# Optimization experiments

Hardware: AMD Instinct MI355X
Metric: run time of the kernel (lower is better)

The kernel has to match this reference:

```python
import jax, jax.numpy as jnp
import numpy as np

N = 100000   # nodes
E = 600000   # edges
B = 512      # graphs in batch
H = 128      # hidden dim
ED = 8       # edge feature dim
TWO48 = float(2 ** 48 - 1)


def _w(k, shape, fan_in):
    return jax.random.normal(k, shape, jnp.float32) * (1.0 / np.sqrt(fan_in))


def setup_inputs() -> dict:
    key = jax.random.key(0)
    ks = jax.random.split(key, 32)
    inp = {}
    inp["s_node_ids"] = jax.random.randint(ks[0], (N,), 0, 2 ** 31 - 1, dtype=jnp.int32)
    inp["s_edge_index"] = jax.random.randint(ks[1], (2, E), 0, N, dtype=jnp.int32)
    inp["s_edge_attr"] = jax.random.normal(ks[2], (E, ED), jnp.float32)
    inp["s_batch"] = jnp.sort(jax.random.randint(ks[3], (N,), 0, B, dtype=jnp.int32))
    inp["depth"] = jax.random.uniform(ks[4], (B,), jnp.float32)
    # id_mlp: Linear(1,H) -> ReLU -> Linear(H,H)
    inp["id_w1"] = _w(ks[5], (1, H), 1); inp["id_b1"] = jnp.zeros((H,), jnp.float32)
    inp["id_w2"] = _w(ks[6], (H, H), H); inp["id_b2"] = jnp.zeros((H,), jnp.float32)
    # edge_mlp: Linear(ED,H) -> ReLU -> Linear(H,H)
    inp["ed_w1"] = _w(ks[7], (ED, H), ED); inp["ed_b1"] = jnp.zeros((H,), jnp.float32)
    inp["ed_w2"] = _w(ks[8], (H, H), H); inp["ed_b2"] = jnp.zeros((H,), jnp.float32)
    # GINEConv nn MLPs: Linear(H,H) -> ReLU -> Linear(H,H)
    inp["c1_w1"] = _w(ks[9], (H, H), H); inp["c1_b1"] = jnp.zeros((H,), jnp.float32)
    inp["c1_w2"] = _w(ks[10], (H, H), H); inp["c1_b2"] = jnp.zeros((H,), jnp.float32)
    inp["c2_w1"] = _w(ks[11], (H, H), H); inp["c2_b1"] = jnp.zeros((H,), jnp.float32)
    inp["c2_w2"] = _w(ks[12], (H, H), H); inp["c2_b2"] = jnp.zeros((H,), jnp.float32)
    inp["rg_w1"] = _w(ks[13], (H + 1, H), H + 1); inp["rg_b1"] = jnp.zeros((H,), jnp.float32)
    inp["rg_w2"] = _w(ks[14], (H, 1), H); inp["rg_b2"] = jnp.zeros((1,), jnp.float32)
    return inp


def _mlp2(x, w1, b1, w2, b2):
    return jax.nn.relu(x @ w1 + b1) @ w2 + b2


def _gine(x, src, dst, e, w1, b1, w2, b2):
    # message = ReLU(x_j + e), sum-aggregated at dst; out = nn((1+eps)*x + aggr), eps=0
    msg = jax.nn.relu(x[src] + e)                       # [E, H]
    aggr = jax.ops.segment_sum(msg, dst, num_segments=N)  # [N, H]
    return _mlp2(x + aggr, w1, b1, w2, b2)


def _global_mean(x, batch):
    sums = jax.ops.segment_sum(x, batch, num_segments=B)                          # [B, H]
    cnts = jax.ops.segment_sum(jnp.ones((x.shape[0], 1), x.dtype), batch, num_segments=B)
    return sums / jnp.maximum(cnts, 1.0)


def reference(s_node_ids, s_edge_index, s_edge_attr, s_batch, depth,
              id_w1, id_b1, id_w2, id_b2,
              ed_w1, ed_b1, ed_w2, ed_b2,
              c1_w1, c1_b1, c1_w2, c1_b2,
              c2_w1, c2_b1, c2_w2, c2_b2,
              rg_w1, rg_b1, rg_w2, rg_b2):
    src, dst = s_edge_index[0], s_edge_index[1]
    x0 = jnp.clip(s_node_ids.astype(jnp.float32) / TWO48, 0.0, 1.0)[:, None]  # [N,1]
    x = _mlp2(x0, id_w1, id_b1, id_w2, id_b2)                                 # [N,H]
    e = _mlp2(s_edge_attr, ed_w1, ed_b1, ed_w2, ed_b2)                        # [E,H]
    x = jax.nn.relu(_gine(x, src, dst, e, c1_w1, c1_b1, c1_w2, c1_b2))
    x = jax.nn.relu(_gine(x, src, dst, e, c2_w1, c2_b1, c2_w2, c2_b2))
    rep = jnp.concatenate([_global_mean(x, s_batch), depth[:, None]], axis=1)  # [B,H+1]
    return _mlp2(rep, rg_w1, rg_b1, rg_w2, rg_b2)[:, 0]                        # [B]
```

## Files before the change

### kernel.cpp

```cpp
#include <hip/hip_runtime.h>
#include <hip/hip_bf16.h>

#define N_NODES 100000
#define N_EDGES 600000
#define NB      512
#define H       128
#define ED      8
#define SCAN_CHUNK 1024
#define N_CHUNKS   98

typedef __attribute__((ext_vector_type(8))) short short8;
typedef __attribute__((ext_vector_type(4))) float f32x4;
typedef __attribute__((ext_vector_type(4))) unsigned int u32x4;
typedef unsigned short u16;
typedef unsigned int   u32;

static __device__ __forceinline__ u16 f2bf(float f) {
    u32 u = __float_as_uint(f);
    u32 r = u + 0x7fffu + ((u >> 16) & 1u);
    return (u16)(r >> 16);
}
static __device__ __forceinline__ float bf2f(u32 h) {
    return __uint_as_float(h << 16);
}
static __device__ __forceinline__ u32 bfpack(float lo, float hi) {
    u32 r;
    asm("v_cvt_pk_bf16_f32 %0, %1, %2" : "=v"(r) : "v"(lo), "v"(hi));
    return r;
}

__global__ __launch_bounds__(256) void pack_hist_kernel(
    const float* __restrict__ W0, const float* __restrict__ W1,
    const float* __restrict__ W2, const float* __restrict__ W3,
    const float* __restrict__ W4, const float* __restrict__ W5,
    const float* __restrict__ W6,
    short8* __restrict__ O0, short8* __restrict__ O1,
    short8* __restrict__ O2, short8* __restrict__ O3,
    short8* __restrict__ O4, short8* __restrict__ O5,
    short8* __restrict__ O6,
    const int* __restrict__ edge_index, int* __restrict__ counts)
{
    if (blockIdx.x >= 50) {
        int e = (blockIdx.x - 50) * 256 + threadIdx.x;
        if (e < N_EDGES) atomicAdd(&counts[edge_index[N_EDGES + e]], 1);
        return;
    }
    int gid = blockIdx.x * 256 + threadIdx.x;
    const float* W; short8* O; int Krows, kkmax, slot;
    if (gid < 512) { W = W0; O = O0; Krows = ED; kkmax = 1; slot = gid; }
    else {
        int m = (gid - 512) / 2048;
        slot = (gid - 512) % 2048;
        Krows = H; kkmax = 4;
        switch (m) {
            case 0: W = W1; O = O1; break;
            case 1: W = W2; O = O2; break;
            case 2: W = W3; O = O3; break;
            case 3: W = W4; O = O4; break;
            case 4: W = W5; O = O5; break;
            default: W = W6; O = O6; break;
        }
    }
    int lane = slot & 63;
    int t = slot >> 6;
    int nt = t & 1; t >>= 1;
    int kk = t % kkmax;
    int w  = t / kkmax;
    int quad = lane >> 4, n15 = lane & 15;
    int n = w * 32 + nt * 16 + n15;
    short8 v;
    #pragma unroll
    for (int j = 0; j < 8; j++) {
        int k = kk * 32 + quad * 8 + j;
        v[j] = (k < Krows) ? (short)f2bf(W[k * H + n]) : (short)0;
    }
    O[slot] = v;
}

__global__ __launch_bounds__(256) void scan_node_kernel(
    const int* __restrict__ counts, int* __restrict__ chunk_scan,
    int* __restrict__ bsum_raw,
    const int* __restrict__ ids,
    const float* __restrict__ w1, const float* __restrict__ b1,
    const short8* __restrict__ pW2, const float* __restrict__ b2,
    u16* __restrict__ x_out)
{
    __shared__ u16 sH[64 * 136];
    __shared__ float s_x0[64];
    __shared__ int sS[256];
    int tid = threadIdx.x;

    if (blockIdx.x < N_CHUNKS) {
        int base = blockIdx.x * SCAN_CHUNK + tid * 4;
        int4 v = *(const int4*)&counts[base];
        int q0 = v.x, q1 = q0 + v.y, q2 = q1 + v.z, q3 = q2 + v.w;
        sS[tid] = q3;
        __syncthreads();
        #pragma unroll
        for (int off = 1; off < 256; off <<= 1) {
            int t = (tid >= off) ? sS[tid - off] : 0;
            __syncthreads();
            sS[tid] += t;
            __syncthreads();
        }
        int excl = sS[tid] - q3;
        int4 o;
        o.x = excl; o.y = excl + q0; o.z = excl + q1; o.w = excl + q2;
        *(int4*)&chunk_scan[base] = o;
        if (tid == 255) bsum_raw[blockIdx.x] = sS[255];
        return;
    }

    int bid = blockIdx.x - N_CHUNKS;
    int w = tid >> 6, lane = tid & 63, quad = lane >> 4, n15 = lane & 15;
    short8 fW2[4][2];
    #pragma unroll
    for (int kk = 0; kk < 4; kk++) {
        fW2[kk][0] = pW2[((w * 4 + kk) * 2 + 0) * 64 + lane];
        fW2[kk][1] = pW2[((w * 4 + kk) * 2 + 1) * 64 + lane];
    }
    float rb2[2] = { b2[w * 32 + n15], b2[w * 32 + 16 + n15] };
    float w1c = w1[tid & 127], b1c = b1[tid & 127];
    const int ntile = (N_NODES + 63) / 64;
    for (int tile = bid; tile < ntile; tile += 768) {
        int row0 = tile * 64;
        if (tid < 64) {
            int n = row0 + tid;
            float x0 = (n < N_NODES) ? (float)ids[n] / 281474976710655.0f : 0.0f;
            s_x0[tid] = fminf(fmaxf(x0, 0.0f), 1.0f);
        }
        __syncthreads();
        int half = tid >> 7, c = tid & 127;
        #pragma unroll
        for (int rr = 0; rr < 32; rr += 2) {
            int r = half + rr * 2;
            u32 p = bfpack(fmaxf(s_x0[r] * w1c + b1c, 0.0f),
                           fmaxf(s_x0[r + 2] * w1c + b1c, 0.0f));
            sH[r * 136 + c]       = (u16)p;
            sH[(r + 2) * 136 + c] = (u16)(p >> 16);
        }
        __syncthreads();
        f32x4 acc[4][2];
        #pragma unroll
        for (int s = 0; s < 4; s++) { acc[s][0] = (f32x4){0,0,0,0}; acc[s][1] = (f32x4){0,0,0,0}; }
        #pragma unroll
        for (int kk = 0; kk < 4; kk++) {
            #pragma unroll
            for (int s = 0; s < 4; s++) {
                short8 a = *(const short8*)&sH[(s * 16 + n15) * 136 + kk * 32 + quad * 8];
                acc[s][0] = __builtin_amdgcn_mfma_f32_16x16x32_bf16(a, fW2[kk][0], acc[s][0], 0, 0, 0);
                acc[s][1] = __builtin_amdgcn_mfma_f32_16x16x32_bf16(a, fW2[kk][1], acc[s][1], 0, 0, 0);
            }
        }
        __syncthreads();
        #pragma unroll
        for (int s = 0; s < 4; s++)
            #pragma unroll
            for (int nt = 0; nt < 2; nt++) {
                int col = w * 32 + nt * 16 + n15;
                int rb = (s * 16 + quad * 4) * 136 + col;
                u32 p0 = bfpack(acc[s][nt][0] + rb2[nt], acc[s][nt][1] + rb2[nt]);
                u32 p1 = bfpack(acc[s][nt][2] + rb2[nt], acc[s][nt][3] + rb2[nt]);
                sH[rb]       = (u16)p0;
                sH[rb + 136] = (u16)(p0 >> 16);
                sH[rb + 272] = (u16)p1;
                sH[rb + 408] = (u16)(p1 >> 16);
            }
        __syncthreads();
        for (int idx = tid; idx < 64 * 16; idx += 256) {
            int r = idx >> 4, c8 = (idx & 15) << 3;
            int n = row0 + r;
            if (n < N_NODES)
                *(uint4*)&x_out[(long)n * H + c8] = *(const uint4*)&sH[r * 136 + c8];
        }
        __syncthreads();
    }
}

__global__ __launch_bounds__(256) void fill_kernel(
    const int* __restrict__ edge_index,
    const int* __restrict__ chunk_scan, const int* __restrict__ bsum_raw,
    int* __restrict__ counts, int* __restrict__ src_list,
    const float* __restrict__ attr, u16* __restrict__ attr_perm)
{
    __shared__ int sB[128];
    int tid = threadIdx.x;
    int v0 = 0;
    if (tid < 128) {
        v0 = (tid < N_CHUNKS) ? bsum_raw[tid] : 0;
        sB[tid] = v0;
    }
    __syncthreads();
    #pragma unroll
    for (int off = 1; off < 128; off <<= 1) {
        int t = (tid < 128 && tid >= off) ? sB[tid - off] : 0;
        __syncthreads();
        if (tid < 128) sB[tid] += t;
        __syncthreads();
    }
    if (tid < 128) sB[tid] -= v0;
    __syncthreads();

    int e = blockIdx.x * 256 + tid;
    if (e >= N_EDGES) return;
    int src = edge_index[e];
    int dst = edge_index[N_EDGES + e];
    int slot = atomicAdd(&counts[dst], -1) - 1;
    int pos = chunk_scan[dst] + sB[dst >> 10] + slot;
    src_list[pos] = src;
    float4 a0 = *(const float4*)&attr[(long)e * ED];
    float4 a1 = *(const float4*)&attr[(long)e * ED + 4];
    u32 w0 = bfpack(a0.x, a0.y);
    u32 w1 = bfpack(a0.z, a0.w);
    u32 w2 = bfpack(a1.x, a1.y);
    u32 w3 = bfpack(a1.z, a1.w);
    *(uint4*)&attr_perm[(long)pos * ED] = make_uint4(w0, w1, w2, w3);
}

__global__ __launch_bounds__(256) void edge_mlp_mfma(
    const u16* __restrict__ attr_perm,
    const int* __restrict__ chunk_scan, const int* __restrict__ bsum_raw,
    int* __restrict__ row_start,
    const short8* __restrict__ pW1, const float* __restrict__ b1,
    const short8* __restrict__ pW2, const float* __restrict__ b2,
    u16* __restrict__ e_perm)
{
    __shared__ u16 sH[64 * 136];
    __shared__ int sB[128];
    int tid = threadIdx.x;

    if (blockIdx.x < 392) {
        int v0 = 0;
        if (tid < 128) {
            v0 = (tid < N_CHUNKS) ? bsum_raw[tid] : 0;
            sB[tid] = v0;
        }
        __syncthreads();
        #pragma unroll
        for (int off = 1; off < 128; off <<= 1) {
            int t = (tid < 128 && tid >= off) ? sB[tid - off] : 0;
            __syncthreads();
            if (tid < 128) sB[tid] += t;
            __syncthreads();
        }
        if (tid < 128) sB[tid] -= v0;
        __syncthreads();
        int i = blockIdx.x * 256 + tid;
        if (i <= N_NODES) row_start[i] = chunk_scan[i] + sB[i >> 10];
        __syncthreads();
    }

    int w = tid >> 6, lane = tid & 63, quad = lane >> 4, n15 = lane & 15;
    short8 fW1[2];
    fW1[0] = pW1[(w * 2 + 0) * 64 + lane];
    fW1[1] = pW1[(w * 2 + 1) * 64 + lane];
    short8 fW2[4][2];
    #pragma unroll
    for (int kk = 0; kk < 4; kk++) {
        fW2[kk][0] = pW2[((w * 4 + kk) * 2 + 0) * 64 + lane];
        fW2[kk][1] = pW2[((w * 4 + kk) * 2 + 1) * 64 + lane];
    }
    float rb1[2] = { b1[w * 32 + n15], b1[w * 32 + 16 + n15] };
    float rb2[2] = { b2[w * 32 + n15], b2[w * 32 + 16 + n15] };
    const short8 zero8 = (short8){0,0,0,0,0,0,0,0};
    const int ntile = N_EDGES / 64;
    for (int tile = blockIdx.x; tile < ntile; tile += gridDim.x) {
        int row0 = tile * 64;
        short8 av[4];
        #pragma unroll
        for (int s = 0; s < 4; s++) {
            av[s] = zero8;
            if (quad == 0)
                av[s] = *(const short8*)&attr_perm[(long)(row0 + s * 16 + n15) * ED];
        }
        f32x4 acc[4][2];
        #pragma unroll
        for (int s = 0; s < 4; s++) { acc[s][0] = (f32x4){0,0,0,0}; acc[s][1] = (f32x4){0,0,0,0}; }
        #pragma unroll
        for (int s = 0; s < 4; s++) {
            acc[s][0] = __builtin_amdgcn_mfma_f32_16x16x32_bf16(av[s], fW1[0], acc[s][0], 0, 0, 0);
            acc[s][1] = __builtin_amdgcn_mfma_f32_16x16x32_bf16(av[s], fW1[1], acc[s][1], 0, 0, 0);
        }
        #pragma unroll
        for (int s = 0; s < 4; s++)
            #pragma unroll
            for (int nt = 0; nt < 2; nt++) {
                int col = w * 32 + nt * 16 + n15;
                int rb = (s * 16 + quad * 4) * 136 + col;
                u32 p0 = bfpack(fmaxf(acc[s][nt][0] + rb1[nt], 0.0f),
                                fmaxf(acc[s][nt][1] + rb1[nt], 0.0f));
                u32 p1 = bfpack(fmaxf(acc[s][nt][2] + rb1[nt], 0.0f),
                                fmaxf(acc[s][nt][3] + rb1[nt], 0.0f));
                sH[rb]       = (u16)p0;
                sH[rb + 136] = (u16)(p0 >> 16);
                sH[rb + 272] = (u16)p1;
                sH[rb + 408] = (u16)(p1 >> 16);
            }
        __syncthreads();
        #pragma unroll
        for (int s = 0; s < 4; s++) { acc[s][0] = (f32x4){0,0,0,0}; acc[s][1] = (f32x4){0,0,0,0}; }
        #pragma unroll
        for (int kk = 0; kk < 4; kk++) {
            #pragma unroll
            for (int s = 0; s < 4; s++) {
                short8 a = *(const short8*)&sH[(s * 16 + n15) * 136 + kk * 32 + quad * 8];
                acc[s][0] = __builtin_amdgcn_mfma_f32_16x16x32_bf16(a, fW2[kk][0], acc[s][0], 0, 0, 0);
                acc[s][1] = __builtin_amdgcn_mfma_f32_16x16x32_bf16(a, fW2[kk][1], acc[s][1], 0, 0, 0);
            }
        }
        __syncthreads();
        #pragma unroll
        for (int s = 0; s < 4; s++)
            #pragma unroll
            for (int nt = 0; nt < 2; nt++) {
                int col = w * 32 + nt * 16 + n15;
                int rb = (s * 16 + quad * 4) * 136 + col;
                u32 p0 = bfpack(acc[s][nt][0] + rb2[nt], acc[s][nt][1] + rb2[nt]);
                u32 p1 = bfpack(acc[s][nt][2] + rb2[nt], acc[s][nt][3] + rb2[nt]);
                sH[rb]       = (u16)p0;
                sH[rb + 136] = (u16)(p0 >> 16);
                sH[rb + 272] = (u16)p1;
                sH[rb + 408] = (u16)(p1 >> 16);
            }
        __syncthreads();
        for (int idx = tid; idx < 64 * 16; idx += 256) {
            int r = idx >> 4, c8 = (idx & 15) << 3;
            *(uint4*)&e_perm[(long)(row0 + r) * H + c8] = *(const uint4*)&sH[r * 136 + c8];
        }
        __syncthreads();
    }
}

static __device__ __forceinline__ void acc8(float* a, u32x4 xv, u32x4 ev) {
    #pragma unroll
    for (int q = 0; q < 4; q++) {
        a[2 * q + 0] += fmaxf(bf2f(xv[q] & 0xffff) + bf2f(ev[q] & 0xffff), 0.0f);
        a[2 * q + 1] += fmaxf(bf2f(xv[q] >> 16)    + bf2f(ev[q] >> 16),    0.0f);
    }
}

__global__ __launch_bounds__(256) void gine_fused(
    const int* __restrict__ row_start,
    const int* __restrict__ src_list,
    const u16* __restrict__ e_perm,
    const u16* __restrict__ x,
    const short8* __restrict__ pW1, const float* __restrict__ b1,
    const short8* __restrict__ pW2, const float* __restrict__ b2,
    u16* __restrict__ x_out,
    const int* __restrict__ batch, float* __restrict__ sums,
    float* __restrict__ cnt, int do_pool)
{
    __shared__ u16 sA[16 * 136];
    __shared__ int sBt[16];
    int tid  = threadIdx.x;
    int lane = tid & 63;
    int l16  = lane & 15;
    int base = lane & 48;
    int fo   = l16 * 8;
    int r    = tid >> 4;
    int n    = blockIdx.x * 16 + r;
    const u16* xb = x + fo;

    if (do_pool && tid < 16) sBt[tid] = batch[blockIdx.x * 16 + tid];

    int beg = row_start[n];
    int end = row_start[n + 1];
    float a[8], b[8];
    #pragma unroll
    for (int q = 0; q < 8; q++) { a[q] = 0.0f; b[q] = 0.0f; }

    for (int j0 = beg; j0 < end; j0 += 16) {
        int m = min(16, end - j0);
        int sv = src_list[j0 + min(l16, m - 1)];
        const u16* ej = e_perm + (long)j0 * H + fo;
        int j = 0;
        for (; j + 2 <= m; j += 2) {
            int s0 = __shfl(sv, base | j);
            int s1 = __shfl(sv, base | (j + 1));
            u32x4 xv0 = *(const u32x4*)(xb + (long)s0 * H);
            u32x4 ev0 = *(const u32x4*)(ej + (long)(j + 0) * H);
            u32x4 xv1 = *(const u32x4*)(xb + (long)s1 * H);
            u32x4 ev1 = *(const u32x4*)(ej + (long)(j + 1) * H);
            acc8(a, xv0, ev0);
            acc8(b, xv1, ev1);
        }
        if (j < m) {
            int s0 = __shfl(sv, base | j);
            u32x4 xv0 = *(const u32x4*)(xb + (long)s0 * H);
            u32x4 ev0 = *(const u32x4*)(ej + (long)j * H);
            acc8(a, xv0, ev0);
        }
    }
    u32x4 xself = *(const u32x4*)(xb + (long)n * H);
    u32x4 xsrow;
    #pragma unroll
    for (int q = 0; q < 4; q++) {
        float o0 = bf2f(xself[q] & 0xffff) + a[2 * q + 0] + b[2 * q + 0];
        float o1 = bf2f(xself[q] >> 16)    + a[2 * q + 1] + b[2 * q + 1];
        xsrow[q] = bfpack(o0, o1);
    }
    *(uint4*)&sA[r * 136 + fo] = *(uint4*)&xsrow;
    __syncthreads();

    int w = tid >> 6, quad = lane >> 4, n15 = l16;
    float rb1[2] = { b1[w * 32 + n15], b1[w * 32 + 16 + n15] };
    float rb2[2] = { b2[w * 32 + n15], b2[w * 32 + 16 + n15] };
    f32x4 acc[2];
    acc[0] = (f32x4){0,0,0,0}; acc[1] = (f32x4){0,0,0,0};
    #pragma unroll
    for (int kk = 0; kk < 4; kk++) {
        short8 av = *(const short8*)&sA[n15 * 136 + kk * 32 + quad * 8];
        short8 w0 = pW1[((w * 4 + kk) * 2 + 0) * 64 + lane];
        short8 w1v = pW1[((w * 4 + kk) * 2 + 1) * 64 + lane];
        acc[0] = __builtin_amdgcn_mfma_f32_16x16x32_bf16(av, w0, acc[0], 0, 0, 0);
        acc[1] = __builtin_amdgcn_mfma_f32_16x16x32_bf16(av, w1v, acc[1], 0, 0, 0);
    }
    __syncthreads();
    #pragma unroll
    for (int nt = 0; nt < 2; nt++) {
        int col = w * 32 + nt * 16 + n15;
        int rb = (quad * 4) * 136 + col;
        u32 p0 = bfpack(fmaxf(acc[nt][0] + rb1[nt], 0.0f),
                        fmaxf(acc[nt][1] + rb1[nt], 0.0f));
        u32 p1 = bfpack(fmaxf(acc[nt][2] + rb1[nt], 0.0f),
                        fmaxf(acc[nt][3] + rb1[nt], 0.0f));
        sA[rb]       = (u16)p0;
        sA[rb + 136] = (u16)(p0 >> 16);
        sA[rb + 272] = (u16)p1;
        sA[rb + 408] = (u16)(p1 >> 16);
    }
    __syncthreads();
    acc[0] = (f32x4){0,0,0,0}; acc[1] = (f32x4){0,0,0,0};
    #pragma unroll
    for (int kk = 0; kk < 4; kk++) {
        short8 av = *(const short8*)&sA[n15 * 136 + kk * 32 + quad * 8];
        short8 w0 = pW2[((w * 4 + kk) * 2 + 0) * 64 + lane];
        short8 w1v = pW2[((w * 4 + kk) * 2 + 1) * 64 + lane];
        acc[0] = __builtin_amdgcn_mfma_f32_16x16x32_bf16(av, w0, acc[0], 0, 0, 0);
        acc[1] = __builtin_amdgcn_mfma_f32_16x16x32_bf16(av, w1v, acc[1], 0, 0, 0);
    }
    __syncthreads();
    #pragma unroll
    for (int nt = 0; nt < 2; nt++) {
        int col = w * 32 + nt * 16 + n15;
        int rb = (quad * 4) * 136 + col;
        u32 p0 = bfpack(fmaxf(acc[nt][0] + rb2[nt], 0.0f),
                        fmaxf(acc[nt][1] + rb2[nt], 0.0f));
        u32 p1 = bfpack(fmaxf(acc[nt][2] + rb2[nt], 0.0f),
                        fmaxf(acc[nt][3] + rb2[nt], 0.0f));
        sA[rb]       = (u16)p0;
        sA[rb + 136] = (u16)(p0 >> 16);
        sA[rb + 272] = (u16)p1;
        sA[rb + 408] = (u16)(p1 >> 16);
    }
    __syncthreads();
    if (!do_pool) {
        int rr = tid >> 4, c8 = (tid & 15) << 3;
        int nn = blockIdx.x * 16 + rr;
        *(uint4*)&x_out[(long)nn * H + c8] = *(const uint4*)&sA[rr * 136 + c8];
    } else {
        if (tid < 128) {
            int c = tid;
            float acc2 = 0.0f;
            int cur = sBt[0];
            #pragma unroll 4
            for (int rr = 0; rr < 16; rr++) {
                int bb = sBt[rr];
                if (bb != cur) {
                    atomicAdd(&sums[cur * H + c], acc2);
                    acc2 = 0.0f; cur = bb;
                }
                acc2 += bf2f((u32)sA[rr * 136 + c]);
            }
            atomicAdd(&sums[cur * H + c], acc2);
        } else if (tid == 128) {
            int cur = sBt[0];
            float cc = 0.0f;
            for (int rr = 0; rr < 16; rr++) {
                int bb = sBt[rr];
                if (bb != cur) {
                    atomicAdd(&cnt[cur], cc);
                    cc = 0.0f; cur = bb;
                }
                cc += 1.0f;
            }
            atomicAdd(&cnt[cur], cc);
        }
    }
}

__global__ __launch_bounds__(128) void regressor_kernel(
    const float* __restrict__ sums, const float* __restrict__ cnt,
    const float* __restrict__ depth,
    const float* __restrict__ w1, const float* __restrict__ b1,
    const float* __restrict__ w2, const float* __restrict__ b2,
    float* __restrict__ out)
{
    __shared__ float s_mean[H];
    __shared__ float s_red[2];
    int b = blockIdx.x;
    int j = threadIdx.x;
    float c = fmaxf(cnt[b], 1.0f);
    s_mean[j] = sums[b * H + j] / c;
    __syncthreads();
    float h = b1[j];
    #pragma unroll 8
    for (int k = 0; k < H; k++) h += s_mean[k] * w1[k * H + j];
    h += depth[b] * w1[H * H + j];
    h = fmaxf(h, 0.0f);
    float p = h * w2[j];
    #pragma unroll
    for (int off = 32; off >= 1; off >>= 1) p += __shfl_down(p, off, 64);
    if ((j & 63) == 0) s_red[j >> 6] = p;
    __syncthreads();
    if (j == 0) out[b] = s_red[0] + s_red[1] + b2[0];
}

extern "C" void kernel_launch(void* const* d_in, const int* in_sizes, int n_in,
                              void* d_out, int out_size, void* d_ws, size_t ws_size,
                              hipStream_t stream)
{
    const int*   ids   = (const int*)  d_in[0];
    const int*   eidx  = (const int*)  d_in[1];
    const float* eattr = (const float*)d_in[2];
    const int*   batch = (const int*)  d_in[3];
    const float* depth = (const float*)d_in[4];
    const float* id_w1 = (const float*)d_in[5];
    const float* id_b1 = (const float*)d_in[6];
    const float* id_w2 = (const float*)d_in[7];
    const float* id_b2 = (const float*)d_in[8];
    const float* ed_w1 = (const float*)d_in[9];
    const float* ed_b1 = (const float*)d_in[10];
    const float* ed_w2 = (const float*)d_in[11];
    const float* ed_b2 = (const float*)d_in[12];
    const float* c1_w1 = (const float*)d_in[13];
    const float* c1_b1 = (const float*)d_in[14];
    const float* c1_w2 = (const float*)d_in[15];
    const float* c1_b2 = (const float*)d_in[16];
    const float* c2_w1 = (const float*)d_in[17];
    const float* c2_b1 = (const float*)d_in[18];
    const float* c2_w2 = (const float*)d_in[19];
    const float* c2_b2 = (const float*)d_in[20];
    const float* rg_w1 = (const float*)d_in[21];
    const float* rg_b1 = (const float*)d_in[22];
    const float* rg_w2 = (const float*)d_in[23];
    const float* rg_b2 = (const float*)d_in[24];

    char* ws = (char*)d_ws;
    u16*   e_buf    = (u16*)  (ws);
    u16*   x_buf    = (u16*)  (ws + 153600000);
    u16*   xs_buf   = (u16*)  (ws + 179200000);
    float* sums_buf = (float*)(ws + 204800000);
    float* cnt_buf  = (float*)(ws + 205062144);
    int*   counts   = (int*)  (ws + 205064192);
    int*   chunk_sc = (int*)  (ws + 205465600);
    int*   bsum_raw = (int*)  (ws + 205867008);
    int*   src_list = (int*)  (ws + 205868032);
    short8* ed_w1p  = (short8*)(ws + 208268032);
    short8* ed_w2p  = (short8*)(ws + 208276224);
    short8* c1_w1p  = (short8*)(ws + 208308992);
    short8* c1_w2p  = (short8*)(ws + 208341760);
    short8* c2_w1p  = (short8*)(ws + 208374528);
    short8* c2_w2p  = (short8*)(ws + 208407296);
    short8* id_w2p  = (short8*)(ws + 208440064);
    int*   row_start = counts;
    u16*   attr_perm = xs_buf;

    hipMemsetAsync(counts, 0, 401408, stream);
    hipMemsetAsync(sums_buf, 0, (size_t)(NB * H + NB) * 4, stream);

    pack_hist_kernel<<<50 + (N_EDGES + 255) / 256, 256, 0, stream>>>(
        ed_w1, ed_w2, c1_w1, c1_w2, c2_w1, c2_w2, id_w2,
        ed_w1p, ed_w2p, c1_w1p, c1_w2p, c2_w1p, c2_w2p, id_w2p,
        eidx, counts);

    scan_node_kernel<<<N_CHUNKS + 768, 256, 0, stream>>>(
        counts, chunk_sc, bsum_raw,
        ids, id_w1, id_b1, id_w2p, id_b2, x_buf);

    fill_kernel<<<(N_EDGES + 255) / 256, 256, 0, stream>>>(
        eidx, chunk_sc, bsum_raw, counts, src_list, eattr, attr_perm);

    edge_mlp_mfma<<<2048, 256, 0, stream>>>(
        attr_perm, chunk_sc, bsum_raw, row_start,
        ed_w1p, ed_b1, ed_w2p, ed_b2, e_buf);

    gine_fused<<<6250, 256, 0, stream>>>(row_start, src_list, e_buf, x_buf,
                                         c1_w1p, c1_b1, c1_w2p, c1_b2, xs_buf,
                                         batch, sums_buf, cnt_buf, 0);
    gine_fused<<<6250, 256, 0, stream>>>(row_start, src_list, e_buf, xs_buf,
                                         c2_w1p, c2_b1, c2_w2p, c2_b2, x_buf,
                                         batch, sums_buf, cnt_buf, 1);

    regressor_kernel<<<NB, 128, 0, stream>>>(sums_buf, cnt_buf, depth,
                                             rg_w1, rg_b1, rg_w2, rg_b2, (float*)d_out);
}
```

Baseline: 358.9 us.

## Fold sums memset into pack kernel, widen grids, vectorize pooling reduction

Removes the separate memset of the pooling sums and count buffers and zeroes them with extra blocks appended to the pack/histogram kernel, saving one launch on the stream. The node-MLP grid grows from 768 to 1563 tile blocks so each block handles one tile, and the edge-MLP grid grows from 2048 to 3125 blocks. The pooling reduction in the second GINE layer now has 64 threads each summing two packed bf16 columns instead of 128 threads each summing one. These are several independent launch-overhead and occupancy tweaks bundled together.

```diff
diff --git a/kernel.cpp b/kernel.cpp
--- a/kernel.cpp
+++ b/kernel.cpp
@@ -38,8 +38,15 @@
     short8* __restrict__ O2, short8* __restrict__ O3,
     short8* __restrict__ O4, short8* __restrict__ O5,
     short8* __restrict__ O6,
-    const int* __restrict__ edge_index, int* __restrict__ counts)
+    const int* __restrict__ edge_index, int* __restrict__ counts,
+    uint4* __restrict__ sums_zero)
 {
+    const int HIST_BLKS = (N_EDGES + 255) / 256;
+    if (blockIdx.x >= 50 + HIST_BLKS) {
+        int idx = (blockIdx.x - 50 - HIST_BLKS) * 256 + threadIdx.x;
+        if (idx < 16512) sums_zero[idx] = make_uint4(0, 0, 0, 0);
+        return;
+    }
     if (blockIdx.x >= 50) {
         int e = (blockIdx.x - 50) * 256 + threadIdx.x;
         if (e < N_EDGES) atomicAdd(&counts[edge_index[N_EDGES + e]], 1);
@@ -122,7 +129,7 @@
     float rb2[2] = { b2[w * 32 + n15], b2[w * 32 + 16 + n15] };
     float w1c = w1[tid & 127], b1c = b1[tid & 127];
     const int ntile = (N_NODES + 63) / 64;
-    for (int tile = bid; tile < ntile; tile += 768) {
+    for (int tile = bid; tile < ntile; tile += 1563) {
         int row0 = tile * 64;
         if (tid < 64) {
             int n = row0 + tid;
@@ -459,23 +466,28 @@
         int nn = blockIdx.x * 16 + rr;
         *(uint4*)&x_out[(long)nn * H + c8] = *(const uint4*)&sA[rr * 136 + c8];
     } else {
-        if (tid < 128) {
-            int c = tid;
-            float acc2 = 0.0f;
+        if (tid < 64) {
+            int c2 = tid * 2;
+            float s0 = 0.0f, s1 = 0.0f;
             int cur = sBt[0];
-            #pragma unroll 4
+            #pragma unroll
             for (int rr = 0; rr < 16; rr++) {
                 int bb = sBt[rr];
                 if (bb != cur) {
-                    atomicAdd(&sums[cur * H + c], acc2);
-                    acc2 = 0.0f; cur = bb;
+                    atomicAdd(&sums[cur * H + c2],     s0);
+                    atomicAdd(&sums[cur * H + c2 + 1], s1);
+                    s0 = s1 = 0.0f; cur = bb;
                 }
-                acc2 += bf2f((u32)sA[rr * 136 + c]);
+                u32 v = *(const u32*)&sA[rr * 136 + c2];
+                s0 += bf2f(v & 0xffff);
+                s1 += bf2f(v >> 16);
             }
-            atomicAdd(&sums[cur * H + c], acc2);
-        } else if (tid == 128) {
+            atomicAdd(&sums[cur * H + c2],     s0);
+            atomicAdd(&sums[cur * H + c2 + 1], s1);
+        } else if (tid == 64) {
             int cur = sBt[0];
             float cc = 0.0f;
+            #pragma unroll
             for (int rr = 0; rr < 16; rr++) {
                 int bb = sBt[rr];
                 if (bb != cur) {
@@ -567,21 +579,21 @@
     u16*   attr_perm = xs_buf;
 
     hipMemsetAsync(counts, 0, 401408, stream);
-    hipMemsetAsync(sums_buf, 0, (size_t)(NB * H + NB) * 4, stream);
-
-    pack_hist_kernel<<<50 + (N_EDGES + 255) / 256, 256, 0, stream>>>(
+
+    const int HIST_BLKS = (N_EDGES + 255) / 256;
+    pack_hist_kernel<<<50 + HIST_BLKS + 65, 256, 0, stream>>>(
         ed_w1, ed_w2, c1_w1, c1_w2, c2_w1, c2_w2, id_w2,
         ed_w1p, ed_w2p, c1_w1p, c1_w2p, c2_w1p, c2_w2p, id_w2p,
-        eidx, counts);
-
-    scan_node_kernel<<<N_CHUNKS + 768, 256, 0, stream>>>(
+        eidx, counts, (uint4*)sums_buf);
+
+    scan_node_kernel<<<N_CHUNKS + 1563, 256, 0, stream>>>(
         counts, chunk_sc, bsum_raw,
         ids, id_w1, id_b1, id_w2p, id_b2, x_buf);
 
     fill_kernel<<<(N_EDGES + 255) / 256, 256, 0, stream>>>(
         eidx, chunk_sc, bsum_raw, counts, src_list, eattr, attr_perm);
 
-    edge_mlp_mfma<<<2048, 256, 0, stream>>>(
+    edge_mlp_mfma<<<3125, 256, 0, stream>>>(
         attr_perm, chunk_sc, bsum_raw, row_start,
         ed_w1p, ed_b1, ed_w2p, ed_b2, e_buf);
 
```

Measured after the change: 360.8 us. Within noise of the previous version (+0.5%).
